# Kernel tuning notes

Measured on AMD Instinct MI355X. Metric: run time of the kernel, lower is better.

Reference implementation:

```python
import jax, jax.numpy as jnp
import numpy as np

GROUP = 8          # weight_group_size
QMAX = 7.0         # 2**(4-1)-1, narrow-range symmetric int4
EPS = 1e-8


def quant_dequant(w):
    """Per-group (size 8, along in_features) symmetric int4 quant-dequant.
    w: [out, in] -> dequantized [out, in]."""
    O, I = w.shape
    wg = w.reshape(O, I // GROUP, GROUP)
    scale = jnp.max(jnp.abs(wg), axis=-1, keepdims=True) / QMAX  # [O, I/G, 1]
    scale = jnp.maximum(scale, EPS)
    q = jnp.clip(jnp.round(wg / scale), -QMAX, QMAX)
    return (q * scale).reshape(O, I)


def setup_inputs() -> dict:
    key = jax.random.key(0)
    kx, kw, kb = jax.random.split(key, 3)
    tokens, din, dout = 8192, 4096, 4096
    x = jax.random.normal(kx, (tokens, din), dtype=jnp.float32)
    weight = jax.random.normal(kw, (dout, din), dtype=jnp.float32) * 0.02
    bias = jax.random.normal(kb, (dout,), dtype=jnp.float32) * 0.01
    return {"x": x, "weight": weight, "bias": bias}


def reference(x, weight, bias):
    w_deq = quant_dequant(weight)                 # [out, in]
    return jnp.dot(x, w_deq.T) + bias             # [tokens, out]
```

## Files before the change

kernel.cpp:

```cpp
#include <hip/hip_runtime.h>
#include <hip/hip_bf16.h>
#include <stdint.h>

typedef __attribute__((ext_vector_type(8))) __bf16 bf16x8;
typedef __attribute__((ext_vector_type(4))) float f32x4;
typedef __attribute__((ext_vector_type(8))) unsigned short ushort8;

typedef const void __attribute__((address_space(1))) gv_t;
typedef void __attribute__((address_space(3))) lv_t;

#define GL16(g, l) __builtin_amdgcn_global_load_lds((gv_t*)(g), (lv_t*)(l), 16, 0, 0)

__device__ __forceinline__ unsigned short f2bf(float f) {
    unsigned int u = __float_as_uint(f);
    u += 0x7fffu + ((u >> 16) & 1u);
    return (unsigned short)(u >> 16);
}

__global__ void __launch_bounds__(256) qdq_weight(const float* __restrict__ w,
                                                  unsigned short* __restrict__ wb,
                                                  int n_groups) {
    int g = blockIdx.x * 256 + threadIdx.x;
    if (g >= n_groups) return;
    const float4* p = (const float4*)w + (size_t)g * 2;
    float4 v0 = p[0], v1 = p[1];
    float t[8] = {v0.x, v0.y, v0.z, v0.w, v1.x, v1.y, v1.z, v1.w};
    float amax = 0.0f;
#pragma unroll
    for (int j = 0; j < 8; ++j) amax = fmaxf(amax, fabsf(t[j]));
    float scale = fmaxf(amax / 7.0f, 1e-8f);
    ushort8 o;
#pragma unroll
    for (int j = 0; j < 8; ++j) {
        float q = rintf(t[j] / scale);
        q = fminf(fmaxf(q, -7.0f), 7.0f);
        o[j] = f2bf(q * scale);
    }
    *((ushort8*)wb + g) = o;
}

__global__ void __launch_bounds__(256) cvt_bf16(const float* __restrict__ x,
                                                unsigned short* __restrict__ xb,
                                                int n8) {
    int i = blockIdx.x * 256 + threadIdx.x;
    if (i >= n8) return;
    const float4* p = (const float4*)x + (size_t)i * 2;
    float4 v0 = p[0], v1 = p[1];
    ushort8 o;
    o[0] = f2bf(v0.x); o[1] = f2bf(v0.y); o[2] = f2bf(v0.z); o[3] = f2bf(v0.w);
    o[4] = f2bf(v1.x); o[5] = f2bf(v1.y); o[6] = f2bf(v1.z); o[7] = f2bf(v1.w);
    *((ushort8*)xb + i) = o;
}

#define BM 256
#define BN 256
#define BK 64

#define MFMA_Q(qm, qn, AF, BF)                                                 \
    __builtin_amdgcn_s_setprio(1);                                             \
    _Pragma("unroll")                                                          \
    for (int mi = 0; mi < 4; ++mi)                                             \
        _Pragma("unroll")                                                      \
        for (int ni = 0; ni < 2; ++ni)                                         \
            _Pragma("unroll")                                                  \
            for (int ks = 0; ks < 2; ++ks)                                     \
                acc[(qm) * 4 + mi][(qn) * 2 + ni] =                            \
                    __builtin_amdgcn_mfma_f32_16x16x32_bf16(                   \
                        AF[mi][ks], BF[ni][ks],                                \
                        acc[(qm) * 4 + mi][(qn) * 2 + ni], 0, 0, 0);           \
    __builtin_amdgcn_s_setprio(0);

#define STAGE_A(b, h, kk)                                                      \
    {                                                                          \
        GL16(gA + (size_t)((h) * 64 + srow) * K + (kk) + schunk,               \
             &sA[b][h][0] + sldso);                                            \
        GL16(gA + (size_t)((h) * 64 + 128 + srow) * K + (kk) + schunk,         \
             &sA[b][h][64 * BK] + sldso);                                      \
    }
#define STAGE_B(b, h, kk)                                                      \
    {                                                                          \
        GL16(gB + (size_t)((h) * 32 + brow) * K + (kk) + schunk,               \
             &sB[b][h][0] + sldso);                                            \
        GL16(gB + (size_t)((h) * 32 + 128 + brow) * K + (kk) + schunk,         \
             &sB[b][h][64 * BK] + sldso);                                      \
    }

#define READ_A(dst, b, h)                                                      \
    _Pragma("unroll")                                                          \
    for (int mi = 0; mi < 4; ++mi) {                                           \
        const int s_ = (wr * 64 + mi * 16 + lr) * BK;                          \
        dst[mi][0] = *(const bf16x8*)&sA[b][h][s_ + e0];                       \
        dst[mi][1] = *(const bf16x8*)&sA[b][h][s_ + e1];                       \
    }
#define READ_B(dst, b, h)                                                      \
    _Pragma("unroll")                                                          \
    for (int ni = 0; ni < 2; ++ni) {                                           \
        const int s_ = (bcol + ni * 16 + lr) * BK;                             \
        dst[ni][0] = *(const bf16x8*)&sB[b][h][s_ + e0];                       \
        dst[ni][1] = *(const bf16x8*)&sB[b][h][s_ + e1];                       \
    }

#define BAR_()     asm volatile("s_barrier" ::: "memory")
#define VM_(n)     asm volatile("s_waitcnt vmcnt(" #n ")" ::: "memory")
#define LGKM_(n)   asm volatile("s_waitcnt lgkmcnt(" #n ")" ::: "memory")
#define SCHEDBAR() __builtin_amdgcn_sched_barrier(0)

#define PHASE(RDS, STG, QM, QN, AF, BF, HINT, VMQ)                             \
    {                                                                          \
        RDS;                                                                   \
        STG;                                                                   \
        HINT;                                                                  \
        BAR_();                                                                \
        LGKM_(0);                                                              \
        SCHEDBAR();                                                            \
        MFMA_Q(QM, QN, AF, BF);                                                \
        VMQ;                                                                   \
        BAR_();                                                                \
    }

__global__ void __launch_bounds__(512, 2)
gemm256(const unsigned short* __restrict__ A,
        const unsigned short* __restrict__ B,
        const float* __restrict__ bias,
        float* __restrict__ C,
        int M, int N, int K) {
    __shared__ unsigned short sA[2][2][128 * BK];
    __shared__ unsigned short sB[2][2][128 * BK];

    const int t  = threadIdx.x;
    const int w  = t >> 6;
    const int ln = t & 63;
    const int lr = ln & 15;
    const int lk = ln >> 4;
    const int wr = w >> 2;
    const int wc = w & 3;
    const int bcol = (wc >> 1) * 64 + (wc & 1) * 32;

    const int nbn = N / BN;
    const int bid = blockIdx.x;
    const int swz = ((int)gridDim.x & 7) ? bid
                  : ((bid & 7) * ((int)gridDim.x >> 3) + (bid >> 3));
    const int m0 = (swz / nbn) * BM;
    const int n0 = (swz % nbn) * BN;

    const unsigned short* gA = A + (size_t)m0 * K;
    const unsigned short* gB = B + (size_t)n0 * K;

    const int srow   = t >> 3;
    const int brow   = (srow & 31) + ((srow >> 5) << 6);
    const int schunk = (((t & 7) ^ (srow & 7)) << 3);
    const int sldso  = (w * 8) * BK;

    const int sw = (lr & 7) << 3;
    const int e0 = (lk * 8) ^ sw;
    const int e1 = (32 + lk * 8) ^ sw;

    f32x4 acc[8][4];
#pragma unroll
    for (int i = 0; i < 8; ++i)
#pragma unroll
        for (int j = 0; j < 4; ++j)
            acc[i][j] = (f32x4)(0.0f);

    const int NT = K / BK;
    const int J  = NT / 2;

    bf16x8 a0f[4][2], a1f[4][2], b0f[2][2], b1f[2][2];

    STAGE_A(0, 0, 0);
    STAGE_B(0, 0, 0);
    STAGE_A(0, 1, 0);
    STAGE_B(0, 1, 0);
    STAGE_A(1, 0, BK);
    STAGE_B(1, 0, BK);
    VM_(4);
    BAR_();

    for (int it = 0; it < J; ++it) {
        const int t0 = 2 * it;
        const int k1 = (t0 + 1) * BK;
        int k2 = (t0 + 2) * BK;  if (k2 >= K) k2 = 0;
        int k3 = (t0 + 3) * BK;  if (k3 >= K) k3 = 0;

        PHASE(READ_A(a0f, 0, 0); READ_B(b0f, 0, 0),
              STAGE_A(1, 1, k1), 0, 0, a0f, b0f, LGKM_(8), );
        PHASE(READ_A(a1f, 0, 1),
              STAGE_B(1, 1, k1), 1, 0, a1f, b0f, , );
        PHASE(READ_B(b1f, 0, 1),
              STAGE_A(0, 0, k2), 1, 1, a1f, b1f, , );
        PHASE(, STAGE_B(0, 0, k2), 0, 1, a0f, b1f, , VM_(4));

        PHASE(READ_A(a0f, 1, 0); READ_B(b0f, 1, 0),
              STAGE_A(0, 1, k2), 0, 0, a0f, b0f, LGKM_(8), );
        PHASE(READ_A(a1f, 1, 1),
              STAGE_B(0, 1, k2), 1, 0, a1f, b0f, , );
        PHASE(READ_B(b1f, 1, 1),
              STAGE_A(1, 0, k3), 1, 1, a1f, b1f, , );
        PHASE(, STAGE_B(1, 0, k3), 0, 1, a0f, b1f, , VM_(4));
    }

#pragma unroll
    for (int j = 0; j < 4; ++j) {
        const int n = n0 + wc * 64 + (j >> 1) * 32 + (j & 1) * 16 + lr;
        const float bv = bias[n];
#pragma unroll
        for (int i = 0; i < 8; ++i) {
            const int m = m0 + wr * 128 + (i >> 2) * 64 + (i & 3) * 16 + lk * 4;
            f32x4 v = acc[i][j];
            C[(size_t)(m + 0) * N + n] = v[0] + bv;
            C[(size_t)(m + 1) * N + n] = v[1] + bv;
            C[(size_t)(m + 2) * N + n] = v[2] + bv;
            C[(size_t)(m + 3) * N + n] = v[3] + bv;
        }
    }
}

extern "C" void kernel_launch(void* const* d_in, const int* in_sizes, int n_in,
                              void* d_out, int out_size, void* d_ws, size_t ws_size,
                              hipStream_t stream) {
    const float* x    = (const float*)d_in[0];
    const float* wgt  = (const float*)d_in[1];
    const float* bias = (const float*)d_in[2];
    float* out        = (float*)d_out;

    const int dout = in_sizes[2];
    const int din  = in_sizes[1] / dout;
    const int M    = in_sizes[0] / din;
    const int N    = dout, K = din;

    unsigned short* xb = (unsigned short*)d_ws;
    unsigned short* wb = xb + (size_t)M * K;

    const int ng_w = (N * K) / 8;
    qdq_weight<<<(ng_w + 255) / 256, 256, 0, stream>>>(wgt, wb, ng_w);

    const int n8_x = (M * K) / 8;
    cvt_bf16<<<(n8_x + 255) / 256, 256, 0, stream>>>(x, xb, n8_x);

    const int nwg = (M / BM) * (N / BN);
    gemm256<<<nwg, 512, 0, stream>>>(xb, wb, bias, out, M, N, K);
}
```

Before: 296.8 us.

## Switch GEMM to 32x32x16 MFMA tiles and fuse prep kernels into one launch

Replaces the 16x16x32 bf16 MFMA inner tiles with 32x32x16 MFMA, changing the LDS fragment read pattern, the accumulator layout (f32x16) and the epilogue store mapping. The larger MFMA shape is meant to cut LDS read traffic and instruction count per FLOP. Separately, the weight quant-dequant and activation bf16 conversion are merged into one kernel launch to save a launch. The new fragment/swizzle indexing risks bank conflicts or layout errors, and the epilogue stores remain strided.

New measurement: 322.2 us. +8.5%, slower.

```diff
diff --git a/kernel.cpp b/kernel.cpp
--- a/kernel.cpp
+++ b/kernel.cpp
@@ -4,6 +4,7 @@
 
 typedef __attribute__((ext_vector_type(8))) __bf16 bf16x8;
 typedef __attribute__((ext_vector_type(4))) float f32x4;
+typedef __attribute__((ext_vector_type(16))) float f32x16;
 typedef __attribute__((ext_vector_type(8))) unsigned short ushort8;
 
 typedef const void __attribute__((address_space(1))) gv_t;
@@ -17,57 +18,54 @@
     return (unsigned short)(u >> 16);
 }
 
-__global__ void __launch_bounds__(256) qdq_weight(const float* __restrict__ w,
-                                                  unsigned short* __restrict__ wb,
-                                                  int n_groups) {
-    int g = blockIdx.x * 256 + threadIdx.x;
-    if (g >= n_groups) return;
-    const float4* p = (const float4*)w + (size_t)g * 2;
-    float4 v0 = p[0], v1 = p[1];
-    float t[8] = {v0.x, v0.y, v0.z, v0.w, v1.x, v1.y, v1.z, v1.w};
-    float amax = 0.0f;
-#pragma unroll
-    for (int j = 0; j < 8; ++j) amax = fmaxf(amax, fabsf(t[j]));
-    float scale = fmaxf(amax / 7.0f, 1e-8f);
-    ushort8 o;
-#pragma unroll
-    for (int j = 0; j < 8; ++j) {
-        float q = rintf(t[j] / scale);
-        q = fminf(fmaxf(q, -7.0f), 7.0f);
-        o[j] = f2bf(q * scale);
-    }
-    *((ushort8*)wb + g) = o;
-}
-
-__global__ void __launch_bounds__(256) cvt_bf16(const float* __restrict__ x,
-                                                unsigned short* __restrict__ xb,
-                                                int n8) {
-    int i = blockIdx.x * 256 + threadIdx.x;
-    if (i >= n8) return;
-    const float4* p = (const float4*)x + (size_t)i * 2;
-    float4 v0 = p[0], v1 = p[1];
-    ushort8 o;
-    o[0] = f2bf(v0.x); o[1] = f2bf(v0.y); o[2] = f2bf(v0.z); o[3] = f2bf(v0.w);
-    o[4] = f2bf(v1.x); o[5] = f2bf(v1.y); o[6] = f2bf(v1.z); o[7] = f2bf(v1.w);
-    *((ushort8*)xb + i) = o;
+__global__ void __launch_bounds__(256) prep(const float* __restrict__ w,
+                                            const float* __restrict__ x,
+                                            unsigned short* __restrict__ wb,
+                                            unsigned short* __restrict__ xb,
+                                            int ng_w, int n8_x) {
+    int id = blockIdx.x * 256 + threadIdx.x;
+    if (id < ng_w) {
+        const float4* p = (const float4*)w + (size_t)id * 2;
+        float4 v0 = p[0], v1 = p[1];
+        float t[8] = {v0.x, v0.y, v0.z, v0.w, v1.x, v1.y, v1.z, v1.w};
+        float amax = 0.0f;
+#pragma unroll
+        for (int j = 0; j < 8; ++j) amax = fmaxf(amax, fabsf(t[j]));
+        float scale = fmaxf(amax / 7.0f, 1e-8f);
+        ushort8 o;
+#pragma unroll
+        for (int j = 0; j < 8; ++j) {
+            float q = rintf(t[j] / scale);
+            q = fminf(fmaxf(q, -7.0f), 7.0f);
+            o[j] = f2bf(q * scale);
+        }
+        *((ushort8*)wb + id) = o;
+    } else {
+        int i = id - ng_w;
+        if (i < n8_x) {
+            const float4* p = (const float4*)x + (size_t)i * 2;
+            float4 v0 = p[0], v1 = p[1];
+            ushort8 o;
+            o[0] = f2bf(v0.x); o[1] = f2bf(v0.y); o[2] = f2bf(v0.z); o[3] = f2bf(v0.w);
+            o[4] = f2bf(v1.x); o[5] = f2bf(v1.y); o[6] = f2bf(v1.z); o[7] = f2bf(v1.w);
+            *((ushort8*)xb + i) = o;
+        }
+    }
 }
 
 #define BM 256
 #define BN 256
 #define BK 64
 
-#define MFMA_Q(qm, qn, AF, BF)                                                 \
+#define MFMA_Q32(qm, qn, AF, BF)                                               \
     __builtin_amdgcn_s_setprio(1);                                             \
     _Pragma("unroll")                                                          \
-    for (int mi = 0; mi < 4; ++mi)                                             \
+    for (int ks = 0; ks < 4; ++ks)                                             \
         _Pragma("unroll")                                                      \
-        for (int ni = 0; ni < 2; ++ni)                                         \
-            _Pragma("unroll")                                                  \
-            for (int ks = 0; ks < 2; ++ks)                                     \
-                acc[(qm) * 4 + mi][(qn) * 2 + ni] =                            \
-                    __builtin_amdgcn_mfma_f32_16x16x32_bf16(                   \
-                        AF[mi][ks], BF[ni][ks],                                \
-                        acc[(qm) * 4 + mi][(qn) * 2 + ni], 0, 0, 0);           \
+        for (int mt = 0; mt < 2; ++mt)                                         \
+            acc[(qm) * 2 + mt][qn] =                                           \
+                __builtin_amdgcn_mfma_f32_32x32x16_bf16(                       \
+                    AF[mt][ks], BF[ks], acc[(qm) * 2 + mt][qn], 0, 0, 0);      \
     __builtin_amdgcn_s_setprio(0);
 
 #define STAGE_A(b, h, kk)                                                      \
@@ -85,20 +83,17 @@
              &sB[b][h][64 * BK] + sldso);                                      \
     }
 
-#define READ_A(dst, b, h)                                                      \
+#define READ_A32(dst, b, h)                                                    \
     _Pragma("unroll")                                                          \
-    for (int mi = 0; mi < 4; ++mi) {                                           \
-        const int s_ = (wr * 64 + mi * 16 + lr) * BK;                          \
-        dst[mi][0] = *(const bf16x8*)&sA[b][h][s_ + e0];                       \
-        dst[mi][1] = *(const bf16x8*)&sA[b][h][s_ + e1];                       \
-    }
-#define READ_B(dst, b, h)                                                      \
+    for (int mt = 0; mt < 2; ++mt)                                             \
+        _Pragma("unroll")                                                      \
+        for (int ks = 0; ks < 4; ++ks)                                         \
+            dst[mt][ks] = *(const bf16x8*)                                     \
+                &sA[b][h][(wr * 64 + mt * 32 + l31) * BK + e32[ks]];
+#define READ_B32(dst, b, h)                                                    \
     _Pragma("unroll")                                                          \
-    for (int ni = 0; ni < 2; ++ni) {                                           \
-        const int s_ = (bcol + ni * 16 + lr) * BK;                             \
-        dst[ni][0] = *(const bf16x8*)&sB[b][h][s_ + e0];                       \
-        dst[ni][1] = *(const bf16x8*)&sB[b][h][s_ + e1];                       \
-    }
+    for (int ks = 0; ks < 4; ++ks)                                             \
+        dst[ks] = *(const bf16x8*)&sB[b][h][(bcol + l31) * BK + e32[ks]];
 
 #define BAR_()     asm volatile("s_barrier" ::: "memory")
 #define VM_(n)     asm volatile("s_waitcnt vmcnt(" #n ")" ::: "memory")
@@ -113,7 +108,7 @@
         BAR_();                                                                \
         LGKM_(0);                                                              \
         SCHEDBAR();                                                            \
-        MFMA_Q(QM, QN, AF, BF);                                                \
+        MFMA_Q32(QM, QN, AF, BF);                                              \
         VMQ;                                                                   \
         BAR_();                                                                \
     }
@@ -127,13 +122,14 @@
     __shared__ unsigned short sA[2][2][128 * BK];
     __shared__ unsigned short sB[2][2][128 * BK];
 
-    const int t  = threadIdx.x;
-    const int w  = t >> 6;
-    const int ln = t & 63;
-    const int lr = ln & 15;
-    const int lk = ln >> 4;
-    const int wr = w >> 2;
-    const int wc = w & 3;
+    const int t   = threadIdx.x;
+    const int w   = t >> 6;
+    const int ln  = t & 63;
+    const int l31 = ln & 31;
+    const int lk5 = ln >> 5;
+    const int l7  = ln & 7;
+    const int wr  = w >> 2;
+    const int wc  = w & 3;
     const int bcol = (wc >> 1) * 64 + (wc & 1) * 32;
 
     const int nbn = N / BN;
@@ -151,21 +147,22 @@
     const int schunk = (((t & 7) ^ (srow & 7)) << 3);
     const int sldso  = (w * 8) * BK;
 
-    const int sw = (lr & 7) << 3;
-    const int e0 = (lk * 8) ^ sw;
-    const int e1 = (32 + lk * 8) ^ sw;
-
-    f32x4 acc[8][4];
-#pragma unroll
-    for (int i = 0; i < 8; ++i)
-#pragma unroll
-        for (int j = 0; j < 4; ++j)
-            acc[i][j] = (f32x4)(0.0f);
+    int e32[4];
+#pragma unroll
+    for (int ks = 0; ks < 4; ++ks)
+        e32[ks] = (((ks * 2 + lk5) ^ l7) << 3);
+
+    f32x16 acc[4][2];
+#pragma unroll
+    for (int i = 0; i < 4; ++i)
+#pragma unroll
+        for (int j = 0; j < 2; ++j)
+            acc[i][j] = (f32x16)(0.0f);
 
     const int NT = K / BK;
     const int J  = NT / 2;
 
-    bf16x8 a0f[4][2], a1f[4][2], b0f[2][2], b1f[2][2];
+    bf16x8 a0f[2][4], a1f[2][4], b0f[4], b1f[4];
 
     STAGE_A(0, 0, 0);
     STAGE_B(0, 0, 0);
@@ -182,35 +179,37 @@
         int k2 = (t0 + 2) * BK;  if (k2 >= K) k2 = 0;
         int k3 = (t0 + 3) * BK;  if (k3 >= K) k3 = 0;
 
-        PHASE(READ_A(a0f, 0, 0); READ_B(b0f, 0, 0),
+        PHASE(READ_A32(a0f, 0, 0); READ_B32(b0f, 0, 0),
               STAGE_A(1, 1, k1), 0, 0, a0f, b0f, LGKM_(8), );
-        PHASE(READ_A(a1f, 0, 1),
+        PHASE(READ_A32(a1f, 0, 1),
               STAGE_B(1, 1, k1), 1, 0, a1f, b0f, , );
-        PHASE(READ_B(b1f, 0, 1),
+        PHASE(READ_B32(b1f, 0, 1),
               STAGE_A(0, 0, k2), 1, 1, a1f, b1f, , );
         PHASE(, STAGE_B(0, 0, k2), 0, 1, a0f, b1f, , VM_(4));
 
-        PHASE(READ_A(a0f, 1, 0); READ_B(b0f, 1, 0),
+        PHASE(READ_A32(a0f, 1, 0); READ_B32(b0f, 1, 0),
               STAGE_A(0, 1, k2), 0, 0, a0f, b0f, LGKM_(8), );
-        PHASE(READ_A(a1f, 1, 1),
+        PHASE(READ_A32(a1f, 1, 1),
               STAGE_B(0, 1, k2), 1, 0, a1f, b0f, , );
-        PHASE(READ_B(b1f, 1, 1),
+        PHASE(READ_B32(b1f, 1, 1),
               STAGE_A(1, 0, k3), 1, 1, a1f, b1f, , );
         PHASE(, STAGE_B(1, 0, k3), 0, 1, a0f, b1f, , VM_(4));
     }
-
-#pragma unroll
-    for (int j = 0; j < 4; ++j) {
-        const int n = n0 + wc * 64 + (j >> 1) * 32 + (j & 1) * 16 + lr;
+    VM_(0);
+
+#pragma unroll
+    for (int qn = 0; qn < 2; ++qn) {
+        const int n = n0 + wc * 64 + qn * 32 + l31;
         const float bv = bias[n];
 #pragma unroll
-        for (int i = 0; i < 8; ++i) {
-            const int m = m0 + wr * 128 + (i >> 2) * 64 + (i & 3) * 16 + lk * 4;
-            f32x4 v = acc[i][j];
-            C[(size_t)(m + 0) * N + n] = v[0] + bv;
-            C[(size_t)(m + 1) * N + n] = v[1] + bv;
-            C[(size_t)(m + 2) * N + n] = v[2] + bv;
-            C[(size_t)(m + 3) * N + n] = v[3] + bv;
+        for (int i = 0; i < 4; ++i) {
+            const int mb = m0 + wr * 128 + (i >> 1) * 64 + (i & 1) * 32 + lk5 * 4;
+            f32x16 v = acc[i][qn];
+#pragma unroll
+            for (int rq = 0; rq < 4; ++rq)
+#pragma unroll
+                for (int rr = 0; rr < 4; ++rr)
+                    C[(size_t)(mb + rq * 8 + rr) * N + n] = v[rq * 4 + rr] + bv;
         }
     }
 }
@@ -232,10 +231,8 @@
     unsigned short* wb = xb + (size_t)M * K;
 
     const int ng_w = (N * K) / 8;
-    qdq_weight<<<(ng_w + 255) / 256, 256, 0, stream>>>(wgt, wb, ng_w);
-
     const int n8_x = (M * K) / 8;
-    cvt_bf16<<<(n8_x + 255) / 256, 256, 0, stream>>>(x, xb, n8_x);
+    prep<<<(ng_w + n8_x + 255) / 256, 256, 0, stream>>>(wgt, x, wb, xb, ng_w, n8_x);
 
     const int nwg = (M / BM) * (N / BN);
     gemm256<<<nwg, 512, 0, stream>>>(xb, wb, bias, out, M, N, K);
```
